# Kernel optimization log

Hardware: AMD Instinct MI355X
Metric: run time of the kernel (lower is better)

## Reference

```python
import jax, jax.numpy as jnp
import numpy as np

M = 4  # block size for overlapped mode
NEG = -1e30  # stands in for -inf; exp(NEG - max) == 0 exactly in fp32


def setup_inputs() -> dict:
    key = jax.random.key(0)
    ks = jax.random.split(key, 8)
    B, T, d, c = 4, 8192, 1024, 128
    return {
        "H": jax.random.normal(ks[0], (B, T, d), dtype=jnp.float32),
        "W_a_KV": jax.random.normal(ks[1], (d, c), dtype=jnp.float32),
        "W_b_KV": jax.random.normal(ks[2], (d, c), dtype=jnp.float32),
        "W_a_Z": jax.random.normal(ks[3], (d, c), dtype=jnp.float32),
        "W_b_Z": jax.random.normal(ks[4], (d, c), dtype=jnp.float32),
        "B_a": jax.random.normal(ks[5], (M, c), dtype=jnp.float32),
        "B_b": jax.random.normal(ks[6], (M, c), dtype=jnp.float32),
    }


def reference(H, W_a_KV, W_b_KV, W_a_Z, W_b_Z, B_a, B_b):
    B, T, d = H.shape
    c = W_a_KV.shape[1]
    nb = T // M  # number of blocks

    # dense projections (cuBLAS-equivalent GEMMs)
    C_a = (H @ W_a_KV).reshape(B, nb, M, c)
    C_b = (H @ W_b_KV).reshape(B, nb, M, c)
    Z_a = (H @ W_a_Z).reshape(B, nb, M, c) + B_a  # bias broadcast over blocks
    Z_b = (H @ W_b_Z).reshape(B, nb, M, c) + B_b

    # block i attends to its own block (a) and the PREVIOUS block (b);
    # block 0 has no previous block -> masked logits / zero values
    Z_b_prev = jnp.concatenate(
        [jnp.full((B, 1, M, c), NEG, dtype=H.dtype), Z_b[:, :-1]], axis=1)
    C_b_prev = jnp.concatenate(
        [jnp.zeros((B, 1, M, c), dtype=H.dtype), C_b[:, :-1]], axis=1)

    logits = jnp.concatenate([Z_a, Z_b_prev], axis=2)   # [B, nb, 2M, c]
    vals = jnp.concatenate([C_a, C_b_prev], axis=2)     # [B, nb, 2M, c]
    probs = jax.nn.softmax(logits, axis=2)              # softmax over 2M window
    return (probs * vals).sum(axis=2)                   # [B, nb, c]
```

## Files before the change

kernel.cpp:

```cpp
#include <hip/hip_runtime.h>
#include <hip/hip_fp16.h>

typedef _Float16 f16;
typedef _Float16 f16x8 __attribute__((ext_vector_type(8)));
typedef float f32x16 __attribute__((ext_vector_type(16)));

#define NEGV (-1e30f)

constexpr int T_    = 8192;
constexpr int BATCH = 4;
constexpr int D_    = 1024;
constexpr int ROWS  = BATCH * T_;
constexpr int BM    = 128;
constexpr int BK    = 64;
constexpr int KT    = D_ / BK;
constexpr int NWG   = ROWS / BM;
constexpr int NTHR  = 512;

#define BOUND_OFF (1u << 20)

__device__ __forceinline__ void gload_lds16(const void* g, void* l) {
  __builtin_amdgcn_global_load_lds(
      (const __attribute__((address_space(1))) void*)g,
      (__attribute__((address_space(3))) void*)l, 16, 0, 0);
}

__global__ __launch_bounds__(1024) void tc_prep(
    const float* __restrict__ H,
    const float* __restrict__ Wakv, const float* __restrict__ Wbkv,
    const float* __restrict__ Waz,  const float* __restrict__ Wbz,
    unsigned char* __restrict__ ws)
{
  const int b = blockIdx.x, t = threadIdx.x;
  if (b < NWG) {
    float* bound = (float*)(ws + BOUND_OFF) + (long long)b * 1024;
    if ((b & 63) == 0) {
      bound[t] = (t < 512) ? 0.f : NEGV;
      return;
    }
    __shared__ float hrow[4][1024];
    __shared__ float part[8][8][128];
    const long long R0 = (long long)b * BM - 4;
    for (int i = t; i < 4096; i += 1024) hrow[i >> 10][i & 1023] = H[R0 * D_ + i];
    __syncthreads();

    const int j  = t & 127;
    const int kc = t >> 7;
    const int k0 = kc * 128;
    float acc[2][4] = {{0.f,0.f,0.f,0.f},{0.f,0.f,0.f,0.f}};
#pragma unroll 4
    for (int k = k0; k < k0 + 128; ++k) {
      const float w0 = Wbkv[k*128 + j];
      const float w1 = Wbz [k*128 + j];
#pragma unroll
      for (int m = 0; m < 4; ++m) {
        const float hv = hrow[m][k];
        acc[0][m] += hv * w0;
        acc[1][m] += hv * w1;
      }
    }
#pragma unroll
    for (int half = 0; half < 2; ++half)
#pragma unroll
      for (int m = 0; m < 4; ++m) part[kc][half*4 + m][j] = acc[half][m];
    __syncthreads();
    {
      const int half = t >> 9, rm = (t >> 7) & 3, jj = t & 127;
      float s = 0.f;
#pragma unroll
      for (int kk = 0; kk < 8; ++kk) s += part[kk][half*4 + rm][jj];
      bound[t] = s;
    }
  } else {
    const int u   = (b - NWG) * 1024 + t;
    const int kt  = u >> 12;
    const int rem = u & 4095;
    const int k8  = rem >> 9;
    const int col = rem & 511;
    const int mat = col >> 7, j = col & 127;
    const float* Wm = (mat == 0) ? Wakv : (mat == 1) ? Wbkv : (mat == 2) ? Waz : Wbz;
    f16x8 v;
#pragma unroll
    for (int e = 0; e < 8; ++e) v[e] = (f16)Wm[(kt*64 + k8*8 + e)*128 + j];
    *(f16x8*)(ws + (size_t)kt*65536 + col*128 + ((k8*16) ^ ((col & 7) << 4))) = v;
  }
}

__global__ __launch_bounds__(NTHR, 2) void tc_main(
    const float* __restrict__ H,
    const float* __restrict__ Ba,
    const float* __restrict__ Bbb,
    const unsigned char* __restrict__ ws,
    float* __restrict__ out)
{
  __shared__ __align__(16) unsigned char lds[163840];

  const int tid  = threadIdx.x;
  const int w    = tid >> 6;
  const int lane = tid & 63;
  const int g    = blockIdx.x;
  const long long R0 = (long long)g * BM;

  f32x16 acc[2][4];
#pragma unroll
  for (int i = 0; i < 2; ++i)
#pragma unroll
    for (int jq = 0; jq < 4; ++jq)
#pragma unroll
      for (int e = 0; e < 16; ++e) acc[i][jq][e] = 0.f;

  const int ar   = tid >> 2;
  const int akq  = tid & 3;
  const float* aptr = H + (R0 + ar) * D_ + akq * 16;
  const int abase = ar * 128;
  const int aswz  = (ar & 7) << 4;

  const int whalf = w >> 2;
  const int jpos  = w & 3;
  const int mrow  = lane & 31;
  const int kq2   = (lane >> 5) * 16;
  const int axor  = (mrow & 7) << 4;
  const int arow0 = (whalf*64 + mrow) * 128;
  const int arow1 = arow0 + 32*128;
  const int jb    = (jpos*32 + mrow) * 128;

  float4 areg[4];
  f16x8 ra0[2], ra1[2], rb[2][4];

#define SA_OFF(IDX) ((IDX) * 16384)
#define SB_OFF(IDX) (32768 + (IDX) * 65536)

#define STAGE_B(KTN, DSTOFF)                                                     \
  { _Pragma("unroll")                                                            \
    for (int r = 0; r < 8; ++r)                                                  \
      gload_lds16(ws + (size_t)(KTN)*65536 + w*1024 + r*8192 + lane*16,          \
                  lds + (DSTOFF) + w*1024 + r*8192); }

#define LOAD_AREG(KTN)                                                           \
  { const float4* p = (const float4*)(aptr + (KTN) * 64);                        \
    areg[0] = p[0]; areg[1] = p[1]; areg[2] = p[2]; areg[3] = p[3]; }

#define WRITE_A(DSTOFF)                                                          \
  { f16x8 v0, v1; const float* af = (const float*)areg;                          \
    _Pragma("unroll")                                                            \
    for (int e = 0; e < 8; ++e) { v0[e] = (f16)af[e]; v1[e] = (f16)af[8 + e]; }  \
    *(f16x8*)(lds + (DSTOFF) + abase + ((akq*32)      ^ aswz)) = v0;             \
    *(f16x8*)(lds + (DSTOFF) + abase + ((akq*32 + 16) ^ aswz)) = v1; }

#define READ_SUBS(SAOFF, SBOFF, KF0)                                             \
  { _Pragma("unroll")                                                            \
    for (int kk = 0; kk < 2; ++kk) {                                             \
      const int ko = ((((KF0) + kk)*32 + kq2) ^ axor);                           \
      ra0[kk] = *(const f16x8*)(lds + (SAOFF) + arow0 + ko);                     \
      ra1[kk] = *(const f16x8*)(lds + (SAOFF) + arow1 + ko);                     \
      _Pragma("unroll")                                                          \
      for (int gr = 0; gr < 4; ++gr)                                             \
        rb[kk][gr] = *(const f16x8*)(lds + (SBOFF) + gr*16384 + jb + ko); } }

#define MFMA_SUBS()                                                              \
  { _Pragma("unroll")                                                            \
    for (int kk = 0; kk < 2; ++kk)                                               \
      _Pragma("unroll")                                                          \
      for (int gr = 0; gr < 4; ++gr) {                                           \
        acc[0][gr] = __builtin_amdgcn_mfma_f32_32x32x16_f16(ra0[kk], rb[kk][gr], acc[0][gr], 0, 0, 0); \
        acc[1][gr] = __builtin_amdgcn_mfma_f32_32x32x16_f16(ra1[kk], rb[kk][gr], acc[1][gr], 0, 0, 0); } }

  LOAD_AREG(0);
  __builtin_amdgcn_sched_barrier(0);
  STAGE_B(0, SB_OFF(0));
  WRITE_A(SA_OFF(0));
  asm volatile("s_waitcnt vmcnt(0) lgkmcnt(0)" ::: "memory");
  __builtin_amdgcn_sched_barrier(0);
  __builtin_amdgcn_s_barrier();

  for (int kt = 0; kt < KT; ++kt) {
    const int cur = kt & 1, nxt = cur ^ 1;
    const int ktn = (kt + 1) & (KT - 1);
    const int saOff = SA_OFF(cur), sbOff = SB_OFF(cur);

    LOAD_AREG(ktn);
    __builtin_amdgcn_sched_barrier(0);
    STAGE_B(ktn, SB_OFF(nxt));
    READ_SUBS(saOff, sbOff, 0);
    __builtin_amdgcn_s_barrier();
    asm volatile("s_waitcnt lgkmcnt(0)" ::: "memory");
    __builtin_amdgcn_sched_barrier(0);
    __builtin_amdgcn_s_setprio(1);
    MFMA_SUBS();
    __builtin_amdgcn_s_setprio(0);
    __builtin_amdgcn_sched_barrier(0);
    __builtin_amdgcn_s_barrier();

    READ_SUBS(saOff, sbOff, 2);
    WRITE_A(SA_OFF(nxt));
    asm volatile("s_waitcnt vmcnt(0) lgkmcnt(0)" ::: "memory");
    __builtin_amdgcn_sched_barrier(0);
    __builtin_amdgcn_s_barrier();
    __builtin_amdgcn_sched_barrier(0);
    __builtin_amdgcn_s_setprio(1);
    MFMA_SUBS();
    __builtin_amdgcn_s_setprio(0);
    __builtin_amdgcn_sched_barrier(0);
    __builtin_amdgcn_s_barrier();
  }

  float* eCb = (float*)lds;
  float* eZb = (float*)(lds + 65536);
  const int jj = jpos*32 + mrow;
  const int h  = lane >> 5;

#pragma unroll
  for (int rf = 0; rf < 2; ++rf)
#pragma unroll
    for (int r = 0; r < 16; ++r) {
      const int row = whalf*64 + rf*32 + (r & 3) + 8*(r >> 2) + 4*h;
      eCb[row*128 + jj] = acc[rf][1][r];
      eZb[row*128 + jj] = acc[rf][3][r];
    }
  __syncthreads();

  float bav[4], bbv[4];
#pragma unroll
  for (int m = 0; m < 4; ++m) { bav[m] = Ba[m*128 + jj]; bbv[m] = Bbb[m*128 + jj]; }
  const float* bound = (const float*)(ws + BOUND_OFF) + (long long)g * 1024;

#pragma unroll
  for (int rf = 0; rf < 2; ++rf)
#pragma unroll
    for (int q = 0; q < 4; ++q) {
      const int bf = 2*q + h;
      const int bl = whalf*16 + rf*8 + bf;
      float za[4], ca[4], zb[4], cb[4];
#pragma unroll
      for (int m = 0; m < 4; ++m) {
        za[m] = acc[rf][2][q*4 + m] + bav[m];
        ca[m] = acc[rf][0][q*4 + m];
      }
      if (bl == 0) {
#pragma unroll
        for (int m = 0; m < 4; ++m) {
          cb[m] = bound[m*128 + jj];
          zb[m] = bound[512 + m*128 + jj] + bbv[m];
        }
      } else {
#pragma unroll
        for (int m = 0; m < 4; ++m) {
          const int pr = bl*4 - 4 + m;
          cb[m] = eCb[pr*128 + jj];
          zb[m] = eZb[pr*128 + jj] + bbv[m];
        }
      }
      float mx = za[0];
#pragma unroll
      for (int m = 1; m < 4; ++m) mx = fmaxf(mx, za[m]);
#pragma unroll
      for (int m = 0; m < 4; ++m) mx = fmaxf(mx, zb[m]);
      float s = 0.f, o = 0.f;
#pragma unroll
      for (int m = 0; m < 4; ++m) {
        const float ea = __expf(za[m] - mx);
        const float eb = __expf(zb[m] - mx);
        s += ea + eb;
        o += ea*ca[m] + eb*cb[m];
      }
      out[((long long)g*32 + bl)*128 + jj] = o / s;
    }
}

extern "C" void kernel_launch(void* const* d_in, const int* in_sizes, int n_in,
                              void* d_out, int out_size, void* d_ws, size_t ws_size,
                              hipStream_t stream) {
  const float* H    = (const float*)d_in[0];
  const float* Wakv = (const float*)d_in[1];
  const float* Wbkv = (const float*)d_in[2];
  const float* Waz  = (const float*)d_in[3];
  const float* Wbz  = (const float*)d_in[4];
  const float* Ba   = (const float*)d_in[5];
  const float* Bbb  = (const float*)d_in[6];
  float* out        = (float*)d_out;
  unsigned char* ws = (unsigned char*)d_ws;

  tc_prep<<<NWG + 64, 1024, 0, stream>>>(H, Wakv, Wbkv, Waz, Wbz, ws);
  tc_main<<<NWG, NTHR, 0, stream>>>(H, Ba, Bbb, ws, out);
}
```

Baseline: 78.16 us.

## Restructure GEMM main loop into four-phase pipeline with double-buffered A registers

```diff
diff --git a/kernel.cpp b/kernel.cpp
--- a/kernel.cpp
+++ b/kernel.cpp
@@ -124,85 +124,97 @@
   const int arow1 = arow0 + 32*128;
   const int jb    = (jpos*32 + mrow) * 128;
 
-  float4 areg[4];
-  f16x8 ra0[2], ra1[2], rb[2][4];
+  float4 areg0[4], areg1[4];
+  f16x8 ra0, ra1, rb0, rb1, rb2, rb3;
 
 #define SA_OFF(IDX) ((IDX) * 16384)
 #define SB_OFF(IDX) (32768 + (IDX) * 65536)
 
-#define STAGE_B(KTN, DSTOFF)                                                     \
+#define STAGE_B4(KTN, DSTOFF, RBASE)                                             \
   { _Pragma("unroll")                                                            \
-    for (int r = 0; r < 8; ++r)                                                  \
+    for (int r = (RBASE); r < (RBASE) + 4; ++r)                                  \
       gload_lds16(ws + (size_t)(KTN)*65536 + w*1024 + r*8192 + lane*16,          \
                   lds + (DSTOFF) + w*1024 + r*8192); }
 
-#define LOAD_AREG(KTN)                                                           \
+#define LOAD_AREG(KTN, A)                                                        \
   { const float4* p = (const float4*)(aptr + (KTN) * 64);                        \
-    areg[0] = p[0]; areg[1] = p[1]; areg[2] = p[2]; areg[3] = p[3]; }
-
-#define WRITE_A(DSTOFF)                                                          \
-  { f16x8 v0, v1; const float* af = (const float*)areg;                          \
+    A[0] = p[0]; A[1] = p[1]; A[2] = p[2]; A[3] = p[3]; }
+
+#define WRITE_A(DSTOFF, A)                                                       \
+  { f16x8 v0, v1; const float* af = (const float*)A;                             \
     _Pragma("unroll")                                                            \
     for (int e = 0; e < 8; ++e) { v0[e] = (f16)af[e]; v1[e] = (f16)af[8 + e]; }  \
     *(f16x8*)(lds + (DSTOFF) + abase + ((akq*32)      ^ aswz)) = v0;             \
     *(f16x8*)(lds + (DSTOFF) + abase + ((akq*32 + 16) ^ aswz)) = v1; }
 
-#define READ_SUBS(SAOFF, SBOFF, KF0)                                             \
-  { _Pragma("unroll")                                                            \
-    for (int kk = 0; kk < 2; ++kk) {                                             \
-      const int ko = ((((KF0) + kk)*32 + kq2) ^ axor);                           \
-      ra0[kk] = *(const f16x8*)(lds + (SAOFF) + arow0 + ko);                     \
-      ra1[kk] = *(const f16x8*)(lds + (SAOFF) + arow1 + ko);                     \
-      _Pragma("unroll")                                                          \
-      for (int gr = 0; gr < 4; ++gr)                                             \
-        rb[kk][gr] = *(const f16x8*)(lds + (SBOFF) + gr*16384 + jb + ko); } }
-
-#define MFMA_SUBS()                                                              \
-  { _Pragma("unroll")                                                            \
-    for (int kk = 0; kk < 2; ++kk)                                               \
-      _Pragma("unroll")                                                          \
-      for (int gr = 0; gr < 4; ++gr) {                                           \
-        acc[0][gr] = __builtin_amdgcn_mfma_f32_32x32x16_f16(ra0[kk], rb[kk][gr], acc[0][gr], 0, 0, 0); \
-        acc[1][gr] = __builtin_amdgcn_mfma_f32_32x32x16_f16(ra1[kk], rb[kk][gr], acc[1][gr], 0, 0, 0); } }
-
-  LOAD_AREG(0);
+#define READ_SUB(SAOFF, SBOFF, P)                                                \
+  { const int ko = (((P)*32 + kq2) ^ axor);                                      \
+    ra0 = *(const f16x8*)(lds + (SAOFF) + arow0 + ko);                           \
+    ra1 = *(const f16x8*)(lds + (SAOFF) + arow1 + ko);                           \
+    rb0 = *(const f16x8*)(lds + (SBOFF) + 0*16384 + jb + ko);                    \
+    rb1 = *(const f16x8*)(lds + (SBOFF) + 1*16384 + jb + ko);                    \
+    rb2 = *(const f16x8*)(lds + (SBOFF) + 2*16384 + jb + ko);                    \
+    rb3 = *(const f16x8*)(lds + (SBOFF) + 3*16384 + jb + ko); }
+
+#define MFMA_SUB()                                                               \
+  { acc[0][0] = __builtin_amdgcn_mfma_f32_32x32x16_f16(ra0, rb0, acc[0][0], 0,0,0); \
+    acc[1][0] = __builtin_amdgcn_mfma_f32_32x32x16_f16(ra1, rb0, acc[1][0], 0,0,0); \
+    acc[0][1] = __builtin_amdgcn_mfma_f32_32x32x16_f16(ra0, rb1, acc[0][1], 0,0,0); \
+    acc[1][1] = __builtin_amdgcn_mfma_f32_32x32x16_f16(ra1, rb1, acc[1][1], 0,0,0); \
+    acc[0][2] = __builtin_amdgcn_mfma_f32_32x32x16_f16(ra0, rb2, acc[0][2], 0,0,0); \
+    acc[1][2] = __builtin_amdgcn_mfma_f32_32x32x16_f16(ra1, rb2, acc[1][2], 0,0,0); \
+    acc[0][3] = __builtin_amdgcn_mfma_f32_32x32x16_f16(ra0, rb3, acc[0][3], 0,0,0); \
+    acc[1][3] = __builtin_amdgcn_mfma_f32_32x32x16_f16(ra1, rb3, acc[1][3], 0,0,0); }
+
+#define PHASE_TAIL()                                                             \
+  __builtin_amdgcn_sched_barrier(0);                                             \
+  __builtin_amdgcn_s_barrier();                                                  \
+  asm volatile("s_waitcnt lgkmcnt(0)" ::: "memory");                             \
+  __builtin_amdgcn_sched_barrier(0);                                             \
+  __builtin_amdgcn_s_setprio(1)
+
+#define PHASE_END()                                                              \
+  __builtin_amdgcn_s_setprio(0);                                                 \
+  __builtin_amdgcn_sched_barrier(0);                                             \
+  __builtin_amdgcn_s_barrier();                                                  \
+  __builtin_amdgcn_sched_barrier(0)
+
+#define KSTEP(SAC, SBC, SAN, SBN, KTN, KT2, AL, AW)                              \
+  READ_SUB(SAC, SBC, 0);                                                         \
+  STAGE_B4(KTN, SBN, 0);                                                         \
+  PHASE_TAIL(); MFMA_SUB(); PHASE_END();                                         \
+  READ_SUB(SAC, SBC, 1);                                                         \
+  STAGE_B4(KTN, SBN, 4);                                                         \
+  PHASE_TAIL(); MFMA_SUB(); PHASE_END();                                         \
+  READ_SUB(SAC, SBC, 2);                                                         \
+  LOAD_AREG(KT2, AL);                                                            \
+  PHASE_TAIL(); MFMA_SUB(); PHASE_END();                                         \
+  READ_SUB(SAC, SBC, 3);                                                         \
+  WRITE_A(SAN, AW);                                                              \
+  asm volatile("s_waitcnt vmcnt(4)" ::: "memory");                               \
+  PHASE_TAIL(); MFMA_SUB(); PHASE_END()
+
+  LOAD_AREG(0, areg0);
   __builtin_amdgcn_sched_barrier(0);
-  STAGE_B(0, SB_OFF(0));
-  WRITE_A(SA_OFF(0));
-  asm volatile("s_waitcnt vmcnt(0) lgkmcnt(0)" ::: "memory");
+  STAGE_B4(0, SB_OFF(0), 0);
+  STAGE_B4(0, SB_OFF(0), 4);
+  WRITE_A(SA_OFF(0), areg0);
+  LOAD_AREG(1, areg1);
+  asm volatile("s_waitcnt vmcnt(4) lgkmcnt(0)" ::: "memory");
   __builtin_amdgcn_sched_barrier(0);
   __builtin_amdgcn_s_barrier();
-
-  for (int kt = 0; kt < KT; ++kt) {
-    const int cur = kt & 1, nxt = cur ^ 1;
-    const int ktn = (kt + 1) & (KT - 1);
-    const int saOff = SA_OFF(cur), sbOff = SB_OFF(cur);
-
-    LOAD_AREG(ktn);
-    __builtin_amdgcn_sched_barrier(0);
-    STAGE_B(ktn, SB_OFF(nxt));
-    READ_SUBS(saOff, sbOff, 0);
-    __builtin_amdgcn_s_barrier();
-    asm volatile("s_waitcnt lgkmcnt(0)" ::: "memory");
-    __builtin_amdgcn_sched_barrier(0);
-    __builtin_amdgcn_s_setprio(1);
-    MFMA_SUBS();
-    __builtin_amdgcn_s_setprio(0);
-    __builtin_amdgcn_sched_barrier(0);
-    __builtin_amdgcn_s_barrier();
-
-    READ_SUBS(saOff, sbOff, 2);
-    WRITE_A(SA_OFF(nxt));
-    asm volatile("s_waitcnt vmcnt(0) lgkmcnt(0)" ::: "memory");
-    __builtin_amdgcn_sched_barrier(0);
-    __builtin_amdgcn_s_barrier();
-    __builtin_amdgcn_sched_barrier(0);
-    __builtin_amdgcn_s_setprio(1);
-    MFMA_SUBS();
-    __builtin_amdgcn_s_setprio(0);
-    __builtin_amdgcn_sched_barrier(0);
-    __builtin_amdgcn_s_barrier();
+  __builtin_amdgcn_sched_barrier(0);
+
+  for (int kt = 0; kt < KT; kt += 2) {
+    const int ktn  = kt + 1;
+    const int kt2  = (kt + 2) & (KT - 1);
+    const int kt3  = (kt + 3) & (KT - 1);
+    KSTEP(SA_OFF(0), SB_OFF(0), SA_OFF(1), SB_OFF(1), ktn, kt2, areg0, areg1);
+    KSTEP(SA_OFF(1), SB_OFF(1), SA_OFF(0), SB_OFF(0), kt2, kt3, areg1, areg0);
   }
+
+  asm volatile("s_waitcnt vmcnt(0)" ::: "memory");
+  __builtin_amdgcn_s_barrier();
 
   float* eCb = (float*)lds;
   float* eZb = (float*)(lds + 65536);
```

After: 69.39 us. 1.13x faster.

## Halve GEMM tile to 64 rows with single-buffered B and deeper A prefetch

Applied to the files above, without the earlier changes.

```diff
diff --git a/kernel.cpp b/kernel.cpp
--- a/kernel.cpp
+++ b/kernel.cpp
@@ -7,15 +7,13 @@
 
 #define NEGV (-1e30f)
 
-constexpr int T_    = 8192;
-constexpr int BATCH = 4;
 constexpr int D_    = 1024;
-constexpr int ROWS  = BATCH * T_;
-constexpr int BM    = 128;
+constexpr int ROWS  = 32768;
+constexpr int BM    = 64;
 constexpr int BK    = 64;
 constexpr int KT    = D_ / BK;
 constexpr int NWG   = ROWS / BM;
-constexpr int NTHR  = 512;
+constexpr int NTHR  = 256;
 
 #define BOUND_OFF (1u << 20)
 
@@ -34,7 +32,7 @@
   const int b = blockIdx.x, t = threadIdx.x;
   if (b < NWG) {
     float* bound = (float*)(ws + BOUND_OFF) + (long long)b * 1024;
-    if ((b & 63) == 0) {
+    if ((b & 127) == 0) {
       bound[t] = (t < 512) ? 0.f : NEGV;
       return;
     }
@@ -93,7 +91,7 @@
     const unsigned char* __restrict__ ws,
     float* __restrict__ out)
 {
-  __shared__ __align__(16) unsigned char lds[163840];
+  __shared__ __align__(16) unsigned char lds[81920];
 
   const int tid  = threadIdx.x;
   const int w    = tid >> 6;
@@ -115,26 +113,23 @@
   const int abase = ar * 128;
   const int aswz  = (ar & 7) << 4;
 
-  const int whalf = w >> 2;
-  const int jpos  = w & 3;
   const int mrow  = lane & 31;
   const int kq2   = (lane >> 5) * 16;
   const int axor  = (mrow & 7) << 4;
-  const int arow0 = (whalf*64 + mrow) * 128;
+  const int arow0 = mrow * 128;
   const int arow1 = arow0 + 32*128;
-  const int jb    = (jpos*32 + mrow) * 128;
+  const int jb    = (w*32 + mrow) * 128;
 
   float4 areg[4];
-  f16x8 ra0[2], ra1[2], rb[2][4];
-
-#define SA_OFF(IDX) ((IDX) * 16384)
-#define SB_OFF(IDX) (32768 + (IDX) * 65536)
-
-#define STAGE_B(KTN, DSTOFF)                                                     \
+
+#define AOFF(IDX) ((IDX) * 8192)
+#define BOFF 16384
+
+#define STAGE_B(KTN)                                                             \
   { _Pragma("unroll")                                                            \
-    for (int r = 0; r < 8; ++r)                                                  \
-      gload_lds16(ws + (size_t)(KTN)*65536 + w*1024 + r*8192 + lane*16,          \
-                  lds + (DSTOFF) + w*1024 + r*8192); }
+    for (int i = 0; i < 16; ++i)                                                 \
+      gload_lds16(ws + (size_t)(KTN)*65536 + tid*16 + i*4096,                    \
+                  lds + BOFF + tid*16 + i*4096); }
 
 #define LOAD_AREG(KTN)                                                           \
   { const float4* p = (const float4*)(aptr + (KTN) * 64);                        \
@@ -147,73 +142,59 @@
     *(f16x8*)(lds + (DSTOFF) + abase + ((akq*32)      ^ aswz)) = v0;             \
     *(f16x8*)(lds + (DSTOFF) + abase + ((akq*32 + 16) ^ aswz)) = v1; }
 
-#define READ_SUBS(SAOFF, SBOFF, KF0)                                             \
+#define COMPUTE_STEP(SAOFF)                                                      \
   { _Pragma("unroll")                                                            \
-    for (int kk = 0; kk < 2; ++kk) {                                             \
-      const int ko = ((((KF0) + kk)*32 + kq2) ^ axor);                           \
-      ra0[kk] = *(const f16x8*)(lds + (SAOFF) + arow0 + ko);                     \
-      ra1[kk] = *(const f16x8*)(lds + (SAOFF) + arow1 + ko);                     \
-      _Pragma("unroll")                                                          \
-      for (int gr = 0; gr < 4; ++gr)                                             \
-        rb[kk][gr] = *(const f16x8*)(lds + (SBOFF) + gr*16384 + jb + ko); } }
-
-#define MFMA_SUBS()                                                              \
-  { _Pragma("unroll")                                                            \
-    for (int kk = 0; kk < 2; ++kk)                                               \
+    for (int kf = 0; kf < 4; ++kf) {                                             \
+      const int ko = ((kf*32 + kq2) ^ axor);                                     \
+      f16x8 a0 = *(const f16x8*)(lds + (SAOFF) + arow0 + ko);                    \
+      f16x8 a1 = *(const f16x8*)(lds + (SAOFF) + arow1 + ko);                    \
       _Pragma("unroll")                                                          \
       for (int gr = 0; gr < 4; ++gr) {                                           \
-        acc[0][gr] = __builtin_amdgcn_mfma_f32_32x32x16_f16(ra0[kk], rb[kk][gr], acc[0][gr], 0, 0, 0); \
-        acc[1][gr] = __builtin_amdgcn_mfma_f32_32x32x16_f16(ra1[kk], rb[kk][gr], acc[1][gr], 0, 0, 0); } }
+        f16x8 bv = *(const f16x8*)(lds + BOFF + gr*16384 + jb + ko);             \
+        acc[0][gr] = __builtin_amdgcn_mfma_f32_32x32x16_f16(a0, bv, acc[0][gr], 0,0,0); \
+        acc[1][gr] = __builtin_amdgcn_mfma_f32_32x32x16_f16(a1, bv, acc[1][gr], 0,0,0); } } }
 
   LOAD_AREG(0);
   __builtin_amdgcn_sched_barrier(0);
-  STAGE_B(0, SB_OFF(0));
-  WRITE_A(SA_OFF(0));
-  asm volatile("s_waitcnt vmcnt(0) lgkmcnt(0)" ::: "memory");
+  STAGE_B(0);
+  WRITE_A(AOFF(0));
+  LOAD_AREG(1);
+  __builtin_amdgcn_sched_barrier(0);
+  asm volatile("s_waitcnt vmcnt(4) lgkmcnt(0)" ::: "memory");
   __builtin_amdgcn_sched_barrier(0);
   __builtin_amdgcn_s_barrier();
+  __builtin_amdgcn_sched_barrier(0);
 
   for (int kt = 0; kt < KT; ++kt) {
     const int cur = kt & 1, nxt = cur ^ 1;
-    const int ktn = (kt + 1) & (KT - 1);
-    const int saOff = SA_OFF(cur), sbOff = SB_OFF(cur);
-
-    LOAD_AREG(ktn);
-    __builtin_amdgcn_sched_barrier(0);
-    STAGE_B(ktn, SB_OFF(nxt));
-    READ_SUBS(saOff, sbOff, 0);
+    COMPUTE_STEP(AOFF(cur));
+    WRITE_A(AOFF(nxt));
+    __builtin_amdgcn_sched_barrier(0);
+    asm volatile("s_waitcnt lgkmcnt(0)" ::: "memory");
     __builtin_amdgcn_s_barrier();
-    asm volatile("s_waitcnt lgkmcnt(0)" ::: "memory");
-    __builtin_amdgcn_sched_barrier(0);
-    __builtin_amdgcn_s_setprio(1);
-    MFMA_SUBS();
-    __builtin_amdgcn_s_setprio(0);
+    __builtin_amdgcn_sched_barrier(0);
+    STAGE_B((kt + 1) & (KT - 1));
+    LOAD_AREG((kt + 2) & (KT - 1));
+    __builtin_amdgcn_sched_barrier(0);
+    asm volatile("s_waitcnt vmcnt(4)" ::: "memory");
     __builtin_amdgcn_sched_barrier(0);
     __builtin_amdgcn_s_barrier();
-
-    READ_SUBS(saOff, sbOff, 2);
-    WRITE_A(SA_OFF(nxt));
-    asm volatile("s_waitcnt vmcnt(0) lgkmcnt(0)" ::: "memory");
-    __builtin_amdgcn_sched_barrier(0);
-    __builtin_amdgcn_s_barrier();
-    __builtin_amdgcn_sched_barrier(0);
-    __builtin_amdgcn_s_setprio(1);
-    MFMA_SUBS();
-    __builtin_amdgcn_s_setprio(0);
-    __builtin_amdgcn_sched_barrier(0);
-    __builtin_amdgcn_s_barrier();
+    __builtin_amdgcn_sched_barrier(0);
   }
 
+  asm volatile("s_waitcnt vmcnt(0) lgkmcnt(0)" ::: "memory");
+  __builtin_amdgcn_s_barrier();
+
   float* eCb = (float*)lds;
-  float* eZb = (float*)(lds + 65536);
-  const int jj = jpos*32 + mrow;
+  float* eZb = (float*)(lds + 32768);
+  const int jj = w*32 + mrow;
   const int h  = lane >> 5;
 
 #pragma unroll
   for (int rf = 0; rf < 2; ++rf)
 #pragma unroll
     for (int r = 0; r < 16; ++r) {
-      const int row = whalf*64 + rf*32 + (r & 3) + 8*(r >> 2) + 4*h;
+      const int row = rf*32 + (r & 3) + 8*(r >> 2) + 4*h;
       eCb[row*128 + jj] = acc[rf][1][r];
       eZb[row*128 + jj] = acc[rf][3][r];
     }
@@ -228,8 +209,7 @@
   for (int rf = 0; rf < 2; ++rf)
 #pragma unroll
     for (int q = 0; q < 4; ++q) {
-      const int bf = 2*q + h;
-      const int bl = whalf*16 + rf*8 + bf;
+      const int bl = rf*8 + 2*q + h;
       float za[4], ca[4], zb[4], cb[4];
 #pragma unroll
       for (int m = 0; m < 4; ++m) {
@@ -263,7 +243,7 @@
         s += ea + eb;
         o += ea*ca[m] + eb*cb[m];
       }
-      out[((long long)g*32 + bl)*128 + jj] = o / s;
+      out[((long long)g*16 + bl)*128 + jj] = o / s;
     }
 }
 
```

Result: slower. 87.71 us (+12.2%).
